# Kernel optimization log

Hardware: AMD Instinct MI355X
Metric: run time of the kernel (lower is better)

The kernel has to match this reference:

```python
import jax, jax.numpy as jnp
import numpy as np
from jax import lax

GAMMA = 0.05
W_BITS = 16
WF_BITS = 14
SHAPE = (4096, 8192)


def setup_inputs() -> dict:
    key = jax.random.key(0)
    k1, k2 = jax.random.split(key)
    x = jax.random.uniform(k1, SHAPE, dtype=jnp.float32)  # weights in [0,1) -> int part < 2**WF_BITS
    noise_n = jax.random.normal(k2, SHAPE, dtype=jnp.float32)  # replaces torch.randn_like(x)
    return {"x": x, "noise_n": noise_n}


def _sigma(x):
    # weight_int = int(x * 2**wf_bits), truncation toward zero (matches torch .to(int))
    # int32 is sufficient: values < 2**16, sum of squared bit weights < 2**28
    w_int = (x * jnp.float32(2 ** WF_BITS)).astype(jnp.int32)

    def cond(carry):
        w, acc, i = carry
        # original: while weight_int.max() > 0, raising if i > 2**w_bits
        return (jnp.max(w) > 0) & (i <= jnp.int32(2 ** W_BITS))

    def body(carry):
        w, acc, i = carry
        bit = i * (w % 2)          # i * LSB  (floor-mod, matches torch %)
        acc = acc + bit * bit      # binary_comps_sq += binary_rep ** 2
        return (w // 2, acc, i * 2)

    acc0 = jnp.zeros_like(w_int)
    _, acc, _ = lax.while_loop(cond, body, (w_int, acc0, jnp.int32(1)))
    # sigma = gamma * sqrt(sum_k (2^k * bit_k)^2) / 2**wf_bits
    return jnp.float32(GAMMA) * jnp.sqrt(acc.astype(jnp.float32)) / jnp.float32(2 ** WF_BITS)


def reference(x, noise_n):
    return noise_n * _sigma(x)
```

## Files before the change

### kernel.cpp

```cpp
#include <hip/hip_runtime.h>
#include <hip/hip_bf16.h>


__device__ __forceinline__ float sigma_of(float x) {
    unsigned w = (unsigned)(int)(x * 16384.0f);
    unsigned a = w;
    a = (a | (a << 8)) & 0x00FF00FFu;
    a = (a | (a << 4)) & 0x0F0F0F0Fu;
    a = (a | (a << 2)) & 0x33333333u;
    a = (a | (a << 1)) & 0x55555555u;
    return (0.05f * sqrtf((float)a)) * (1.0f / 16384.0f);
}

__global__ __launch_bounds__(256) void weight_noise_kernel(
    const float4* __restrict__ x4,
    const float4* __restrict__ n4,
    float4* __restrict__ o4,
    int count4)
{
    int i = blockIdx.x * blockDim.x + threadIdx.x;
    if (i < count4) {
        float4 xv = x4[i];
        float4 nv = n4[i];
        float4 ov;
        ov.x = nv.x * sigma_of(xv.x);
        ov.y = nv.y * sigma_of(xv.y);
        ov.z = nv.z * sigma_of(xv.z);
        ov.w = nv.w * sigma_of(xv.w);
        o4[i] = ov;
    }
}

extern "C" void kernel_launch(void* const* d_in, const int* in_sizes, int n_in,
                              void* d_out, int out_size, void* d_ws, size_t ws_size,
                              hipStream_t stream) {
    const float4* x4 = (const float4*)d_in[0];
    const float4* nz = (const float4*)d_in[1];
    float4* out = (float4*)d_out;
    int n = in_sizes[0];
    int count4 = n / 4;
    int block = 256;
    int grid = (count4 + block - 1) / block;
    weight_noise_kernel<<<grid, block, 0, stream>>>(x4, nz, out, count4);
}
```

Before: 301.1 us.

## Use grid-stride loop with 4x unrolled loads and nontemporal stores

Caps the grid at 2048 blocks and switches to a grid-stride loop in which each thread issues four independent float4 loads of each input before computing. Outputs are written with nontemporal stores so the streamed output does not pollute the cache. The goal is more memory-level parallelism and less block-launch overhead for a purely bandwidth-bound elementwise op. The risk is that a capped grid leaves fewer waves in flight to hide latency on a large GPU.

```diff
diff --git a/kernel.cpp b/kernel.cpp
--- a/kernel.cpp
+++ b/kernel.cpp
@@ -1,6 +1,7 @@
 #include <hip/hip_runtime.h>
-#include <hip/hip_bf16.h>
 
+
+typedef float f4 __attribute__((ext_vector_type(4)));
 
 __device__ __forceinline__ float sigma_of(float x) {
     unsigned w = (unsigned)(int)(x * 16384.0f);
@@ -12,34 +13,53 @@
     return (0.05f * sqrtf((float)a)) * (1.0f / 16384.0f);
 }
 
-__global__ __launch_bounds__(256) void weight_noise_kernel(
-    const float4* __restrict__ x4,
-    const float4* __restrict__ n4,
-    float4* __restrict__ o4,
+__device__ __forceinline__ f4 body(f4 xv, f4 nv) {
+    f4 ov;
+    ov.x = nv.x * sigma_of(xv.x);
+    ov.y = nv.y * sigma_of(xv.y);
+    ov.z = nv.z * sigma_of(xv.z);
+    ov.w = nv.w * sigma_of(xv.w);
+    return ov;
+}
+
+__global__ __launch_bounds__(256, 8) void weight_noise_kernel(
+    const f4* __restrict__ x4,
+    const f4* __restrict__ n4,
+    f4* __restrict__ o4,
     int count4)
 {
+    const int stride = gridDim.x * blockDim.x;
     int i = blockIdx.x * blockDim.x + threadIdx.x;
-    if (i < count4) {
-        float4 xv = x4[i];
-        float4 nv = n4[i];
-        float4 ov;
-        ov.x = nv.x * sigma_of(xv.x);
-        ov.y = nv.y * sigma_of(xv.y);
-        ov.z = nv.z * sigma_of(xv.z);
-        ov.w = nv.w * sigma_of(xv.w);
-        o4[i] = ov;
+
+    for (; i + 3 * stride < count4; i += 4 * stride) {
+        f4 x0 = x4[i];
+        f4 x1 = x4[i + stride];
+        f4 x2 = x4[i + 2 * stride];
+        f4 x3 = x4[i + 3 * stride];
+        f4 n0 = n4[i];
+        f4 n1 = n4[i + stride];
+        f4 n2 = n4[i + 2 * stride];
+        f4 n3 = n4[i + 3 * stride];
+        __builtin_nontemporal_store(body(x0, n0), &o4[i]);
+        __builtin_nontemporal_store(body(x1, n1), &o4[i + stride]);
+        __builtin_nontemporal_store(body(x2, n2), &o4[i + 2 * stride]);
+        __builtin_nontemporal_store(body(x3, n3), &o4[i + 3 * stride]);
+    }
+    for (; i < count4; i += stride) {
+        __builtin_nontemporal_store(body(x4[i], n4[i]), &o4[i]);
     }
 }
 
 extern "C" void kernel_launch(void* const* d_in, const int* in_sizes, int n_in,
                               void* d_out, int out_size, void* d_ws, size_t ws_size,
                               hipStream_t stream) {
-    const float4* x4 = (const float4*)d_in[0];
-    const float4* nz = (const float4*)d_in[1];
-    float4* out = (float4*)d_out;
+    const f4* x4 = (const f4*)d_in[0];
+    const f4* nz = (const f4*)d_in[1];
+    f4* out = (f4*)d_out;
     int n = in_sizes[0];
     int count4 = n / 4;
     int block = 256;
-    int grid = (count4 + block - 1) / block;
+    long long grid_ll = (count4 + block - 1) / block;
+    int grid = (grid_ll > 2048) ? 2048 : (int)grid_ll;
     weight_noise_kernel<<<grid, block, 0, stream>>>(x4, nz, out, count4);
 }
```

New measurement: 327.2 us. 1.09x slower.
